# Optimization experiments

Measured on AMD Instinct MI355X. Metric: run time of the kernel, lower is better.

The kernel has to match this reference:

```python
import jax, jax.numpy as jnp
import numpy as np

S, N, MSA_DIM, PAIR_DIM, D, H = 8, 256, 256, 128, 32, 8
EPS = 1e-5


def layer_norm(x, w, b):
    mu = jnp.mean(x, axis=-1, keepdims=True)
    var = jnp.mean((x - mu) ** 2, axis=-1, keepdims=True)
    return (x - mu) * jax.lax.rsqrt(var + EPS) * w + b


def setup_inputs() -> dict:
    key = jax.random.key(0)
    ks = jax.random.split(key, 8)
    def rnd(k, shape, scale=1.0):
        return jax.random.normal(k, shape, jnp.float32) * scale
    return {
        "msa_rep": rnd(ks[0], (S, N, MSA_DIM)),
        "pair_rep": rnd(ks[1], (N, N, PAIR_DIM)),
        "ln_w": jnp.ones((MSA_DIM,), jnp.float32),
        "ln_b": jnp.zeros((MSA_DIM,), jnp.float32),
        "w_qkv": rnd(ks[2], (MSA_DIM, 3 * H * D), 0.02),
        "ln_pair_w": jnp.ones((PAIR_DIM,), jnp.float32),
        "ln_pair_b": jnp.zeros((PAIR_DIM,), jnp.float32),
        "w_b": rnd(ks[3], (PAIR_DIM, H), 0.02),
        "w_g": rnd(ks[4], (MSA_DIM, H * D), 0.02),
        "w_out": rnd(ks[5], (H * D, MSA_DIM), 0.02),
        "b_out": jnp.zeros((MSA_DIM,), jnp.float32),
    }


def reference(msa_rep, pair_rep, ln_w, ln_b, w_qkv, ln_pair_w, ln_pair_b,
              w_b, w_g, w_out, b_out):
    s, n, _ = msa_rep.shape
    x = layer_norm(msa_rep, ln_w, ln_b)                      # [s, n, msa_dim]
    qkv = x @ w_qkv                                          # [s, n, 3*h*d]
    # chunk(3, dim=-1) then view(..., d, h): d outer, h inner
    q, k, v = [t.reshape(s, n, D, H) for t in jnp.split(qkv, 3, axis=-1)]
    # pair bias: LN + linear -> [n, n, h], broadcast to [1, i, j, 1, h]
    b = layer_norm(pair_rep, ln_pair_w, ln_pair_b) @ w_b     # [n, n, h]
    g = jax.nn.sigmoid(x @ w_g).reshape(s, n, D, H)          # gate [s, n, d, h]
    # NOTE: logits keep the d axis (no contraction): einsum 'sidh,sjdh->sijdh'
    scores = (q[:, :, None, :, :] * k[:, None, :, :, :]) * (D ** -0.5) \
             + b[None, :, :, None, :]                        # [s, i, j, d, h]
    a = jax.nn.softmax(scores, axis=2)                       # softmax over j
    out = g * jnp.einsum('sijdh,sjdh->sidh', a, v)           # [s, n, d, h]
    return out.reshape(s, n, D * H) @ w_out + b_out          # [s, n, msa_dim]
```

## Files before the change

### kernel.cpp

```cpp
#include <hip/hip_runtime.h>
#include <math.h>

#define S_DIM 8
#define N_RES 256
#define MSA_DIM 256
#define PAIR_DIM 128
#define D_DIM 32
#define H_DIM 8
#define M_ROWS (S_DIM * N_RES)
#define QKV_N (3 * H_DIM * D_DIM)
#define HD (H_DIM * D_DIM)
#define XW_N 1024
#define LOG2E 1.4426950408889634f

typedef __attribute__((ext_vector_type(8))) short short8;
typedef __attribute__((ext_vector_type(4))) float floatx4;

#define DPP_ADD(x, ctrl, rmask)                                                \
    x += __int_as_float(__builtin_amdgcn_update_dpp(                           \
        0, __float_as_int(x), (ctrl), (rmask), 0xf, true))

__device__ __forceinline__ float wave_sum63(float x) {
    DPP_ADD(x, 0x111, 0xf);
    DPP_ADD(x, 0x112, 0xf);
    DPP_ADD(x, 0x114, 0xf);
    DPP_ADD(x, 0x118, 0xf);
    DPP_ADD(x, 0x142, 0xa);
    DPP_ADD(x, 0x143, 0xc);
    return x;
}

__device__ __forceinline__ float quad_sum(float x) {
    x += __int_as_float(__builtin_amdgcn_update_dpp(
        0, __float_as_int(x), 0xB1, 0xf, 0xf, true));
    x += __int_as_float(__builtin_amdgcn_update_dpp(
        0, __float_as_int(x), 0x4E, 0xf, 0xf, true));
    return x;
}

__device__ __forceinline__ unsigned short bf16rn(float v) {
    unsigned u = __float_as_uint(v);
    return (unsigned short)((u + 0x7FFF + ((u >> 16) & 1)) >> 16);
}

__global__ __launch_bounds__(256) void prep_kernel(
    const float* __restrict__ w_qkv, const float* __restrict__ w_g,
    unsigned short* __restrict__ whiT, unsigned short* __restrict__ wloT,
    const float* __restrict__ w_out,
    unsigned short* __restrict__ wouthiT, unsigned short* __restrict__ woutloT,
    const float* __restrict__ msa, const float* __restrict__ lnw,
    const float* __restrict__ lnb, unsigned short* __restrict__ xhi,
    unsigned short* __restrict__ xlo)
{
    __shared__ float shm[8];
    int bx = blockIdx.x;
    int t = threadIdx.x;

    if (bx < 2048) {
        int row = bx;
        float v = msa[row * MSA_DIM + t];
        float s1 = wave_sum63(v);
        float s2 = wave_sum63(v * v);
        float* r1 = shm;
        float* r2 = shm + 4;
        int wave = t >> 6, lane = t & 63;
        if (lane == 63) { r1[wave] = s1; r2[wave] = s2; }
        __syncthreads();
        float S1 = r1[0] + r1[1] + r1[2] + r1[3];
        float S2 = r2[0] + r2[1] + r2[2] + r2[3];
        float mu = S1 * (1.0f / 256.0f);
        float var = S2 * (1.0f / 256.0f) - mu * mu;
        float rs = rsqrtf(var + 1e-5f);
        float y = (v - mu) * rs * lnw[t] + lnb[t];
        unsigned short h = bf16rn(y);
        xhi[row * 256 + t] = h;
        xlo[row * 256 + t] = bf16rn(y - __uint_as_float((unsigned)h << 16));
    } else if (bx < 2176) {
        int id = (bx - 2048) * 256 + t;
        int n = id >> 5, oct = id & 31, k0 = oct * 8;
        const float* src;
        int stride;
        if (n < QKV_N) { src = w_qkv + n; stride = QKV_N; }
        else           { src = w_g + (n - QKV_N); stride = HD; }
        unsigned short h8[8], l8[8];
#pragma unroll
        for (int j = 0; j < 8; j++) {
            float v = src[(size_t)(k0 + j) * stride];
            unsigned short h = bf16rn(v);
            h8[j] = h;
            l8[j] = bf16rn(v - __uint_as_float((unsigned)h << 16));
        }
        *(short8*)&whiT[n * 256 + k0] = *(short8*)h8;
        *(short8*)&wloT[n * 256 + k0] = *(short8*)l8;
    } else {
        int id = (bx - 2176) * 256 + t;
        int n = id >> 5, oct = id & 31, k0 = oct * 8;
        unsigned short h8[8], l8[8];
#pragma unroll
        for (int j = 0; j < 8; j++) {
            int k = k0 + j;
            int wrow = (k & 31) * 8 + (k >> 5);
            float v = w_out[(size_t)wrow * 256 + n];
            unsigned short h = bf16rn(v);
            h8[j] = h;
            l8[j] = bf16rn(v - __uint_as_float((unsigned)h << 16));
        }
        *(short8*)&wouthiT[n * 256 + k0] = *(short8*)h8;
        *(short8*)&woutloT[n * 256 + k0] = *(short8*)l8;
    }
}

__global__ __launch_bounds__(256) void mid_kernel(
    const float* __restrict__ pair, const float* __restrict__ lw,
    const float* __restrict__ lb, const float* __restrict__ wb,
    float* __restrict__ b2,
    const unsigned short* __restrict__ xhi, const unsigned short* __restrict__ xlo,
    const unsigned short* __restrict__ whiT, const unsigned short* __restrict__ wloT,
    float* __restrict__ q_t, float* __restrict__ k_t,
    float* __restrict__ v_t, float* __restrict__ g_t)
{
    __shared__ __align__(16) char smem[35840];
    int bx = blockIdx.x;
    int t = threadIdx.x;
    int g3 = bx / 3, r3 = bx - g3 * 3;

    if (r3 != 2) {
        float* As = (float*)smem;
        float* Spart = (float*)smem + 1552;
        float* Qpart = (float*)smem + 1816;
        int pair_id = g3 * 2 + r3;
        if (t < 128) {
            float lwc = lw[t];
#pragma unroll
            for (int h = 0; h < 8; h++)
                As[t * 12 + h] = lwc * wb[t * 8 + h] * LOG2E;
        }
        __syncthreads();
        {
            int h = t >> 5, seg = t & 31, cbase = seg * 4;
            float sa = 0, sq = 0;
#pragma unroll
            for (int cc = 0; cc < 4; cc++) {
                int c = cbase + cc;
                sa += As[c * 12 + h];
                sq += lb[c] * wb[c * 8 + h];
            }
            Spart[h * 33 + seg] = sa;
            Qpart[h * 33 + seg] = sq * LOG2E;
        }
        __syncthreads();
        if (t < 8) {
            float s = 0, q = 0;
#pragma unroll
            for (int j = 0; j < 32; j++) {
                s += Spart[t * 33 + j];
                q += Qpart[t * 33 + j];
            }
            As[1536 + t] = s;
            As[1544 + t] = q;
        }
        __syncthreads();
        int row = pair_id * 64 + (t >> 2);
        int q = t & 3;
        const float* in = pair + (size_t)row * PAIR_DIM;
        float4 x4[8];
#pragma unroll
        for (int it = 0; it < 8; it++)
            x4[it] = *(const float4*)&in[it * 16 + q * 4];
        float s = 0, s2 = 0;
        float dot[8] = {};
#pragma unroll
        for (int it = 0; it < 8; it++) {
            float xk[4];
            *(float4*)xk = x4[it];
#pragma unroll
            for (int k = 0; k < 4; k++) {
                int c = it * 16 + q * 4 + k;
                float xv = xk[k];
                s += xv; s2 += xv * xv;
                float4 A0 = *(const float4*)&As[c * 12];
                float4 A1 = *(const float4*)&As[c * 12 + 4];
                dot[0] += xv * A0.x; dot[1] += xv * A0.y;
                dot[2] += xv * A0.z; dot[3] += xv * A0.w;
                dot[4] += xv * A1.x; dot[5] += xv * A1.y;
                dot[6] += xv * A1.z; dot[7] += xv * A1.w;
            }
        }
        s = quad_sum(s);
        s2 = quad_sum(s2);
#pragma unroll
        for (int h = 0; h < 8; h++) dot[h] = quad_sum(dot[h]);
        float mu = s * (1.0f / 128.0f);
        float var = s2 * (1.0f / 128.0f) - mu * mu;
        float rs = rsqrtf(var + 1e-5f);
        int h0 = q * 2;
#pragma unroll
        for (int u = 0; u < 2; u++) {
            int h = h0 + u;
            b2[h * 65536 + row] = rs * (dot[h] - mu * As[1536 + h]) + As[1544 + h];
        }
    } else {
        unsigned short* As = (unsigned short*)smem;
        unsigned short* Bs = As + 64 * 72;
        float* Cs = (float*)(smem + 18432);
        int gid = g3;
        int n0 = (gid & 15) * 64, m0 = (gid >> 4) * 64;
        int w = t >> 6, L = t & 63;
        int wm = (w & 1) * 32, wn = (w >> 1) * 32;
        int l15 = L & 15, l4 = L >> 4;
        int alm = t >> 3, alk = (t & 7) * 8;
        floatx4 acc[2][2];
#pragma unroll
        for (int a = 0; a < 2; a++)
#pragma unroll
            for (int b = 0; b < 2; b++) acc[a][b] = (floatx4){0, 0, 0, 0};

        short8 pa0 = *(const short8*)&xhi[(m0 + alm) * 256 + alk];
        short8 pa1 = *(const short8*)&xhi[(m0 + alm + 32) * 256 + alk];
        short8 pb[2];
#pragma unroll
        for (int j = 0; j < 2; j++) {
            int id = t + 256 * j;
            int bn = id >> 3, bc = (id & 7) * 8;
            pb[j] = *(const short8*)&whiT[(n0 + bn) * 256 + bc];
        }

        for (int r = 0; r < 12; r++) {
            __syncthreads();
            *(short8*)&As[alm * 72 + alk] = pa0;
            *(short8*)&As[(alm + 32) * 72 + alk] = pa1;
#pragma unroll
            for (int j = 0; j < 2; j++) {
                int id = t + 256 * j;
                int bn = id >> 3, bc = (id & 7) * 8;
                *(short8*)&Bs[bn * 72 + bc] = pb[j];
            }
            __syncthreads();
            if (r < 11) {
                int rn = r + 1;
                int seg = rn >> 2, kb = (rn & 3) * 64;
                const unsigned short* An = (seg == 1) ? xlo : xhi;
                const unsigned short* Bn = (seg == 2) ? wloT : whiT;
                pa0 = *(const short8*)&An[(m0 + alm) * 256 + kb + alk];
                pa1 = *(const short8*)&An[(m0 + alm + 32) * 256 + kb + alk];
#pragma unroll
                for (int j = 0; j < 2; j++) {
                    int id = t + 256 * j;
                    int bn = id >> 3, bc = (id & 7) * 8;
                    pb[j] = *(const short8*)&Bn[(n0 + bn) * 256 + kb + bc];
                }
            }
#pragma unroll
            for (int ks = 0; ks < 2; ks++) {
                int ko = ks * 32 + l4 * 8;
                short8 af[2], bf[2];
#pragma unroll
                for (int a = 0; a < 2; a++)
                    af[a] = *(short8*)&As[(wm + a * 16 + l15) * 72 + ko];
#pragma unroll
                for (int b = 0; b < 2; b++)
                    bf[b] = *(short8*)&Bs[(wn + b * 16 + l15) * 72 + ko];
#pragma unroll
                for (int a = 0; a < 2; a++)
#pragma unroll
                    for (int b = 0; b < 2; b++)
                        acc[a][b] = __builtin_amdgcn_mfma_f32_16x16x32_bf16(
                            af[a], bf[b], acc[a][b], 0, 0, 0);
            }
        }
#pragma unroll
        for (int a = 0; a < 2; a++)
#pragma unroll
            for (int b = 0; b < 2; b++) {
                int nl = wn + b * 16 + l15;
#pragma unroll
                for (int rg = 0; rg < 4; rg++) {
                    int ml = wm + a * 16 + l4 * 4 + rg;
                    Cs[ml * 68 + nl] = acc[a][b][rg];
                }
            }
        __syncthreads();
        int qkv_mode = (n0 < QKV_N);
        int chunk = n0 >> 8;
        int dbase = (n0 & 255) >> 3;
#pragma unroll
        for (int j = 0; j < 4; j++) {
            int id = t + 256 * j;
            int m = id >> 4;
            int h = (id >> 1) & 7;
            int dq = id & 1;
            float vals[4];
#pragma unroll
            for (int jj = 0; jj < 4; jj++)
                vals[jj] = Cs[m * 68 + (dq * 4 + jj) * 8 + h];
            int mm = m0 + m;
            int daddr = dbase + dq * 4;
            if (qkv_mode) {
                float* dst = (chunk == 0) ? q_t : ((chunk == 1) ? k_t : v_t);
                *(float4*)&dst[(size_t)(h * M_ROWS + mm) * D_DIM + daddr] =
                    *(float4*)vals;
            } else {
                float4 o;
                o.x = 1.0f / (1.0f + __expf(-vals[0]));
                o.y = 1.0f / (1.0f + __expf(-vals[1]));
                o.z = 1.0f / (1.0f + __expf(-vals[2]));
                o.w = 1.0f / (1.0f + __expf(-vals[3]));
                *(float4*)&g_t[(size_t)(h * M_ROWS + mm) * D_DIM + daddr] = o;
            }
        }
    }
}

#define KV_STR 40
__global__ __launch_bounds__(256) void attn_kernel(
    const float* __restrict__ q_t, const float* __restrict__ k_t,
    const float* __restrict__ v_t, const float* __restrict__ g_t,
    const float* __restrict__ b2, unsigned short* __restrict__ ao_hi,
    unsigned short* __restrict__ ao_lo)
{
    __shared__ float k_sh[256 * KV_STR];
    __shared__ float v_sh[256 * KV_STR];
    int blk = blockIdx.x;
    int h = blk & 7, s = (blk >> 3) & 7, it = blk >> 6;
    int t = threadIdx.x;
    const float* kb = k_t + (size_t)(h * M_ROWS + s * N_RES) * D_DIM;
    const float* vb = v_t + (size_t)(h * M_ROWS + s * N_RES) * D_DIM;
    for (int idx = t; idx < 2048; idx += 256) {
        int row = idx >> 3, c = (idx & 7) << 2;
        *(float4*)&k_sh[row * KV_STR + c] = ((const float4*)kb)[idx];
        *(float4*)&v_sh[row * KV_STR + c] = ((const float4*)vb)[idx];
    }
    __syncthreads();
    int jp = t & 3, dg = (t >> 2) & 7, li = t >> 5;
    int d0 = dg * 4;
    const float SCL2 = 0.17677669529663687f * LOG2E;
    int ig[4], mrow[4];
    float qs[4][4];
#pragma unroll
    for (int r = 0; r < 4; r++) {
        ig[r] = it * 32 + r * 8 + li;
        mrow[r] = s * N_RES + ig[r];
        float4 q4 = *(const float4*)&q_t[(size_t)(h * M_ROWS + mrow[r]) * D_DIM + d0];
        qs[r][0] = q4.x * SCL2; qs[r][1] = q4.y * SCL2;
        qs[r][2] = q4.z * SCL2; qs[r][3] = q4.w * SCL2;
    }
    float den[4][4] = {}, acc[4][4] = {};
    const float* bbase = b2 + h * 65536;
    for (int js4 = 0; js4 < 16; js4++) {
        float bb[4][4];
#pragma unroll
        for (int r = 0; r < 4; r++)
            *(float4*)&bb[r][0] =
                *(const float4*)&bbase[ig[r] * 256 + jp * 64 + js4 * 4];
#pragma unroll
        for (int u = 0; u < 4; u++) {
            int j = jp * 64 + js4 * 4 + u;
            float ka[4], va[4];
            *(float4*)ka = *(const float4*)&k_sh[j * KV_STR + d0];
            *(float4*)va = *(const float4*)&v_sh[j * KV_STR + d0];
#pragma unroll
            for (int r = 0; r < 4; r++) {
#pragma unroll
                for (int c = 0; c < 4; c++) {
                    float e = __builtin_amdgcn_exp2f(qs[r][c] * ka[c] + bb[r][u]);
                    den[r][c] += e;
                    acc[r][c] += e * va[c];
                }
            }
        }
    }
#pragma unroll
    for (int r = 0; r < 4; r++)
#pragma unroll
        for (int c = 0; c < 4; c++) {
            den[r][c] = quad_sum(den[r][c]);
            acc[r][c] = quad_sum(acc[r][c]);
        }
    if (jp == 0) {
#pragma unroll
        for (int r = 0; r < 4; r++) {
            float4 g4 = *(const float4*)&g_t[(size_t)(h * M_ROWS + mrow[r]) * D_DIM + d0];
            float o[4];
            o[0] = g4.x * acc[r][0] / den[r][0];
            o[1] = g4.y * acc[r][1] / den[r][1];
            o[2] = g4.z * acc[r][2] / den[r][2];
            o[3] = g4.w * acc[r][3] / den[r][3];
            unsigned short hi[4], lo[4];
#pragma unroll
            for (int c = 0; c < 4; c++) {
                hi[c] = bf16rn(o[c]);
                lo[c] = bf16rn(o[c] - __uint_as_float((unsigned)hi[c] << 16));
            }
            size_t base = (size_t)mrow[r] * 256 + h * 32 + d0;
            uint2 ph, pl;
            ph.x = (unsigned)hi[0] | ((unsigned)hi[1] << 16);
            ph.y = (unsigned)hi[2] | ((unsigned)hi[3] << 16);
            pl.x = (unsigned)lo[0] | ((unsigned)lo[1] << 16);
            pl.y = (unsigned)lo[2] | ((unsigned)lo[3] << 16);
            *(uint2*)&ao_hi[base] = ph;
            *(uint2*)&ao_lo[base] = pl;
        }
    }
}

__global__ __launch_bounds__(256) void out_mfma_kernel(
    const unsigned short* __restrict__ ahi, const unsigned short* __restrict__ alo,
    const unsigned short* __restrict__ whi, const unsigned short* __restrict__ wlo,
    const float* __restrict__ bias, float* __restrict__ out)
{
    __shared__ unsigned short As[32 * 72];
    __shared__ unsigned short Bs[64 * 72];
    __shared__ float Cs[32 * 68];
    int t = threadIdx.x;
    int n0 = blockIdx.x * 64, m0 = blockIdx.y * 32;
    int w = t >> 6, L = t & 63;
    int wm = (w & 1) * 16, wn = (w >> 1) * 32;
    int l15 = L & 15, l4 = L >> 4;
    int alm = t >> 3, alk = (t & 7) * 8;
    floatx4 acc[2];
#pragma unroll
    for (int b = 0; b < 2; b++) acc[b] = (floatx4){0, 0, 0, 0};

    short8 pa0 = *(const short8*)&ahi[(m0 + alm) * 256 + alk];
    short8 pb[2];
#pragma unroll
    for (int j = 0; j < 2; j++) {
        int id = t + 256 * j;
        int bn = id >> 3, bc = (id & 7) * 8;
        pb[j] = *(const short8*)&whi[(n0 + bn) * 256 + bc];
    }

    for (int r = 0; r < 12; r++) {
        __syncthreads();
        *(short8*)&As[alm * 72 + alk] = pa0;
#pragma unroll
        for (int j = 0; j < 2; j++) {
            int id = t + 256 * j;
            int bn = id >> 3, bc = (id & 7) * 8;
            *(short8*)&Bs[bn * 72 + bc] = pb[j];
        }
        __syncthreads();
        if (r < 11) {
            int rn = r + 1;
            int seg = rn >> 2, kb = (rn & 3) * 64;
            const unsigned short* An = (seg == 1) ? alo : ahi;
            const unsigned short* Bn = (seg == 2) ? wlo : whi;
            pa0 = *(const short8*)&An[(m0 + alm) * 256 + kb + alk];
#pragma unroll
            for (int j = 0; j < 2; j++) {
                int id = t + 256 * j;
                int bn = id >> 3, bc = (id & 7) * 8;
                pb[j] = *(const short8*)&Bn[(n0 + bn) * 256 + kb + bc];
            }
        }
#pragma unroll
        for (int ks = 0; ks < 2; ks++) {
            int ko = ks * 32 + l4 * 8;
            short8 af, bf[2];
            af = *(short8*)&As[(wm + l15) * 72 + ko];
#pragma unroll
            for (int b = 0; b < 2; b++)
                bf[b] = *(short8*)&Bs[(wn + b * 16 + l15) * 72 + ko];
#pragma unroll
            for (int b = 0; b < 2; b++)
                acc[b] = __builtin_amdgcn_mfma_f32_16x16x32_bf16(
                    af, bf[b], acc[b], 0, 0, 0);
        }
    }
#pragma unroll
    for (int b = 0; b < 2; b++) {
        int nl = wn + b * 16 + l15;
#pragma unroll
        for (int rg = 0; rg < 4; rg++) {
            int ml = wm + l4 * 4 + rg;
            Cs[ml * 68 + nl] = acc[b][rg];
        }
    }
    __syncthreads();
#pragma unroll
    for (int j = 0; j < 2; j++) {
        int id = t + 256 * j;
        int m = id >> 4, nc = (id & 15) * 4;
        float4 v = *(float4*)&Cs[m * 68 + nc];
        float4 bb = *(const float4*)&bias[n0 + nc];
        float4 o;
        o.x = v.x + bb.x; o.y = v.y + bb.y;
        o.z = v.z + bb.z; o.w = v.w + bb.w;
        *(float4*)&out[(size_t)(m0 + m) * 256 + n0 + nc] = o;
    }
}

extern "C" void kernel_launch(void* const* d_in, const int* in_sizes, int n_in,
                              void* d_out, int out_size, void* d_ws, size_t ws_size,
                              hipStream_t stream)
{
    const float* msa_rep   = (const float*)d_in[0];
    const float* pair_rep  = (const float*)d_in[1];
    const float* ln_w      = (const float*)d_in[2];
    const float* ln_b      = (const float*)d_in[3];
    const float* w_qkv     = (const float*)d_in[4];
    const float* ln_pair_w = (const float*)d_in[5];
    const float* ln_pair_b = (const float*)d_in[6];
    const float* w_b       = (const float*)d_in[7];
    const float* w_g       = (const float*)d_in[8];
    const float* w_out     = (const float*)d_in[9];
    const float* b_out     = (const float*)d_in[10];
    float* out = (float*)d_out;

    float* ws = (float*)d_ws;
    const size_t CH = 524288;
    float* q_t = ws + 0 * CH;
    float* k_t = ws + 1 * CH;
    float* v_t = ws + 2 * CH;
    float* g_t = ws + 3 * CH;
    float* b2  = ws + 4 * CH;
    unsigned short* ao_hi   = (unsigned short*)(ws + 5 * CH);
    unsigned short* ao_lo   = ao_hi + (size_t)M_ROWS * 256;
    unsigned short* xhi     = (unsigned short*)(ws + 6 * CH);
    unsigned short* xlo     = xhi + (size_t)M_ROWS * 256;
    unsigned short* whiT    = (unsigned short*)(ws + 7 * CH);
    unsigned short* wloT    = whiT + (size_t)XW_N * 256;
    unsigned short* wouthiT = (unsigned short*)(ws + 8 * CH);
    unsigned short* woutloT = wouthiT + 65536;

    prep_kernel<<<2208, 256, 0, stream>>>(
        w_qkv, w_g, whiT, wloT,
        w_out, wouthiT, woutloT,
        msa_rep, ln_w, ln_b, xhi, xlo);

    mid_kernel<<<1536, 256, 0, stream>>>(
        pair_rep, ln_pair_w, ln_pair_b, w_b, b2,
        xhi, xlo, whiT, wloT, q_t, k_t, v_t, g_t);

    attn_kernel<<<512, 256, 0, stream>>>(q_t, k_t, v_t, g_t, b2, ao_hi, ao_lo);

    out_mfma_kernel<<<dim3(4, 64), 256, 0, stream>>>(
        ao_hi, ao_lo, wouthiT, woutloT, b_out, out);
}
```

Measured before the change: 146.9 us.

## Compact prep kernel to wave-per-row layernorm and drop KV smem padding

The prep kernel now handles one LayerNorm row per wave with float4 loads and readlane broadcasts instead of shared memory and a barrier. It packs the weight transposes into the same 512 blocks using subsets of threads, which cuts the grid from 2208 blocks. The attention kernel drops the padded K/V shared-memory stride in favour of a dense [256][32] layout, and replaces the division with a hardware reciprocal. The dense layout can bring back LDS bank conflicts, and the reciprocal slightly changes precision.

New measurement: 149.2 us. About the same (+1.6%).

```diff
diff --git a/kernel.cpp b/kernel.cpp
--- a/kernel.cpp
+++ b/kernel.cpp
@@ -52,31 +52,46 @@
     const float* __restrict__ lnb, unsigned short* __restrict__ xhi,
     unsigned short* __restrict__ xlo)
 {
-    __shared__ float shm[8];
-    int bx = blockIdx.x;
+    int b = blockIdx.x;
     int t = threadIdx.x;
 
-    if (bx < 2048) {
-        int row = bx;
-        float v = msa[row * MSA_DIM + t];
-        float s1 = wave_sum63(v);
-        float s2 = wave_sum63(v * v);
-        float* r1 = shm;
-        float* r2 = shm + 4;
-        int wave = t >> 6, lane = t & 63;
-        if (lane == 63) { r1[wave] = s1; r2[wave] = s2; }
-        __syncthreads();
-        float S1 = r1[0] + r1[1] + r1[2] + r1[3];
-        float S2 = r2[0] + r2[1] + r2[2] + r2[3];
+    {
+        int wv = t >> 6, l = t & 63;
+        int row = b * 4 + wv;
+        float4 v4 = *(const float4*)&msa[(size_t)row * 256 + l * 4];
+        float s1 = v4.x + v4.y + v4.z + v4.w;
+        float s2 = v4.x * v4.x + v4.y * v4.y + v4.z * v4.z + v4.w * v4.w;
+        s1 = wave_sum63(s1);
+        s2 = wave_sum63(s2);
+        float S1 = __int_as_float(__builtin_amdgcn_readlane(__float_as_int(s1), 63));
+        float S2 = __int_as_float(__builtin_amdgcn_readlane(__float_as_int(s2), 63));
         float mu = S1 * (1.0f / 256.0f);
         float var = S2 * (1.0f / 256.0f) - mu * mu;
         float rs = rsqrtf(var + 1e-5f);
-        float y = (v - mu) * rs * lnw[t] + lnb[t];
-        unsigned short h = bf16rn(y);
-        xhi[row * 256 + t] = h;
-        xlo[row * 256 + t] = bf16rn(y - __uint_as_float((unsigned)h << 16));
-    } else if (bx < 2176) {
-        int id = (bx - 2048) * 256 + t;
+        float4 w4 = *(const float4*)&lnw[l * 4];
+        float4 bb4 = *(const float4*)&lnb[l * 4];
+        float y[4];
+        y[0] = (v4.x - mu) * rs * w4.x + bb4.x;
+        y[1] = (v4.y - mu) * rs * w4.y + bb4.y;
+        y[2] = (v4.z - mu) * rs * w4.z + bb4.z;
+        y[3] = (v4.w - mu) * rs * w4.w + bb4.w;
+        unsigned short hh[4], ll[4];
+#pragma unroll
+        for (int i = 0; i < 4; i++) {
+            hh[i] = bf16rn(y[i]);
+            ll[i] = bf16rn(y[i] - __uint_as_float((unsigned)hh[i] << 16));
+        }
+        uint2 ph, pl;
+        ph.x = (unsigned)hh[0] | ((unsigned)hh[1] << 16);
+        ph.y = (unsigned)hh[2] | ((unsigned)hh[3] << 16);
+        pl.x = (unsigned)ll[0] | ((unsigned)ll[1] << 16);
+        pl.y = (unsigned)ll[2] | ((unsigned)ll[3] << 16);
+        *(uint2*)&xhi[(size_t)row * 256 + l * 4] = ph;
+        *(uint2*)&xlo[(size_t)row * 256 + l * 4] = pl;
+    }
+
+    if (t < 64) {
+        int id = b * 64 + t;
         int n = id >> 5, oct = id & 31, k0 = oct * 8;
         const float* src;
         int stride;
@@ -92,8 +107,8 @@
         }
         *(short8*)&whiT[n * 256 + k0] = *(short8*)h8;
         *(short8*)&wloT[n * 256 + k0] = *(short8*)l8;
-    } else {
-        int id = (bx - 2176) * 256 + t;
+    } else if (t < 80) {
+        int id = b * 16 + (t - 64);
         int n = id >> 5, oct = id & 31, k0 = oct * 8;
         unsigned short h8[8], l8[8];
 #pragma unroll
@@ -213,7 +228,7 @@
 #pragma unroll
         for (int a = 0; a < 2; a++)
 #pragma unroll
-            for (int b = 0; b < 2; b++) acc[a][b] = (floatx4){0, 0, 0, 0};
+            for (int c = 0; c < 2; c++) acc[a][c] = (floatx4){0, 0, 0, 0};
 
         short8 pa0 = *(const short8*)&xhi[(m0 + alm) * 256 + alk];
         short8 pa1 = *(const short8*)&xhi[(m0 + alm + 32) * 256 + alk];
@@ -258,25 +273,25 @@
                 for (int a = 0; a < 2; a++)
                     af[a] = *(short8*)&As[(wm + a * 16 + l15) * 72 + ko];
 #pragma unroll
-                for (int b = 0; b < 2; b++)
-                    bf[b] = *(short8*)&Bs[(wn + b * 16 + l15) * 72 + ko];
+                for (int c = 0; c < 2; c++)
+                    bf[c] = *(short8*)&Bs[(wn + c * 16 + l15) * 72 + ko];
 #pragma unroll
                 for (int a = 0; a < 2; a++)
 #pragma unroll
-                    for (int b = 0; b < 2; b++)
-                        acc[a][b] = __builtin_amdgcn_mfma_f32_16x16x32_bf16(
-                            af[a], bf[b], acc[a][b], 0, 0, 0);
+                    for (int c = 0; c < 2; c++)
+                        acc[a][c] = __builtin_amdgcn_mfma_f32_16x16x32_bf16(
+                            af[a], bf[c], acc[a][c], 0, 0, 0);
             }
         }
 #pragma unroll
         for (int a = 0; a < 2; a++)
 #pragma unroll
-            for (int b = 0; b < 2; b++) {
-                int nl = wn + b * 16 + l15;
+            for (int c = 0; c < 2; c++) {
+                int nl = wn + c * 16 + l15;
 #pragma unroll
                 for (int rg = 0; rg < 4; rg++) {
                     int ml = wm + a * 16 + l4 * 4 + rg;
-                    Cs[ml * 68 + nl] = acc[a][b][rg];
+                    Cs[ml * 68 + nl] = acc[a][c][rg];
                 }
             }
         __syncthreads();
@@ -311,24 +326,22 @@
     }
 }
 
-#define KV_STR 40
 __global__ __launch_bounds__(256) void attn_kernel(
     const float* __restrict__ q_t, const float* __restrict__ k_t,
     const float* __restrict__ v_t, const float* __restrict__ g_t,
     const float* __restrict__ b2, unsigned short* __restrict__ ao_hi,
     unsigned short* __restrict__ ao_lo)
 {
-    __shared__ float k_sh[256 * KV_STR];
-    __shared__ float v_sh[256 * KV_STR];
+    __shared__ float k_sh[256][32];
+    __shared__ float v_sh[256][32];
     int blk = blockIdx.x;
     int h = blk & 7, s = (blk >> 3) & 7, it = blk >> 6;
     int t = threadIdx.x;
     const float* kb = k_t + (size_t)(h * M_ROWS + s * N_RES) * D_DIM;
     const float* vb = v_t + (size_t)(h * M_ROWS + s * N_RES) * D_DIM;
     for (int idx = t; idx < 2048; idx += 256) {
-        int row = idx >> 3, c = (idx & 7) << 2;
-        *(float4*)&k_sh[row * KV_STR + c] = ((const float4*)kb)[idx];
-        *(float4*)&v_sh[row * KV_STR + c] = ((const float4*)vb)[idx];
+        ((float4*)k_sh)[idx] = ((const float4*)kb)[idx];
+        ((float4*)v_sh)[idx] = ((const float4*)vb)[idx];
     }
     __syncthreads();
     int jp = t & 3, dg = (t >> 2) & 7, li = t >> 5;
@@ -356,8 +369,8 @@
         for (int u = 0; u < 4; u++) {
             int j = jp * 64 + js4 * 4 + u;
             float ka[4], va[4];
-            *(float4*)ka = *(const float4*)&k_sh[j * KV_STR + d0];
-            *(float4*)va = *(const float4*)&v_sh[j * KV_STR + d0];
+            *(float4*)ka = *(const float4*)&k_sh[j][d0];
+            *(float4*)va = *(const float4*)&v_sh[j][d0];
 #pragma unroll
             for (int r = 0; r < 4; r++) {
 #pragma unroll
@@ -381,10 +394,10 @@
         for (int r = 0; r < 4; r++) {
             float4 g4 = *(const float4*)&g_t[(size_t)(h * M_ROWS + mrow[r]) * D_DIM + d0];
             float o[4];
-            o[0] = g4.x * acc[r][0] / den[r][0];
-            o[1] = g4.y * acc[r][1] / den[r][1];
-            o[2] = g4.z * acc[r][2] / den[r][2];
-            o[3] = g4.w * acc[r][3] / den[r][3];
+            o[0] = g4.x * acc[r][0] * __builtin_amdgcn_rcpf(den[r][0]);
+            o[1] = g4.y * acc[r][1] * __builtin_amdgcn_rcpf(den[r][1]);
+            o[2] = g4.z * acc[r][2] * __builtin_amdgcn_rcpf(den[r][2]);
+            o[3] = g4.w * acc[r][3] * __builtin_amdgcn_rcpf(den[r][3]);
             unsigned short hi[4], lo[4];
 #pragma unroll
             for (int c = 0; c < 4; c++) {
@@ -523,7 +536,7 @@
     unsigned short* wouthiT = (unsigned short*)(ws + 8 * CH);
     unsigned short* woutloT = wouthiT + 65536;
 
-    prep_kernel<<<2208, 256, 0, stream>>>(
+    prep_kernel<<<512, 256, 0, stream>>>(
         w_qkv, w_g, whiT, wloT,
         w_out, wouthiT, woutloT,
         msa_rep, ln_w, ln_b, xhi, xlo);
```
